# Optimization experiments

Measured on AMD Instinct MI355X. Metric: run time of the kernel, lower is better.

## Reference

```python
import jax, jax.numpy as jnp
import numpy as np
import math

B, S, H, D = 8, 4096, 768, 64  # batch, seq_len, hidden_dim, head_size


def setup_inputs() -> dict:
    key = jax.random.key(0)
    kx, kk, kq, kv, kbk, kbq, kbv = jax.random.split(key, 7)
    s = 1.0 / math.sqrt(H)
    return {
        "x": jax.random.normal(kx, (B, S, H), dtype=jnp.float32),
        "Wk": jax.random.normal(kk, (H, D), dtype=jnp.float32) * s,
        "bk": jax.random.normal(kbk, (D,), dtype=jnp.float32) * s,
        "Wq": jax.random.normal(kq, (H, D), dtype=jnp.float32) * s,
        "bq": jax.random.normal(kbq, (D,), dtype=jnp.float32) * s,
        "Wv": jax.random.normal(kv, (H, D), dtype=jnp.float32) * s,
        "bv": jax.random.normal(kbv, (D,), dtype=jnp.float32) * s,
    }


def reference(x, Wk, bk, Wq, bq, Wv, bv):
    # projections: [B, S, D]
    k = x @ Wk + bk
    q = x @ Wq + bq
    v = x @ Wv + bv
    # full O(S^2) attention scores, as in the original module
    weight = jnp.einsum("bqd,bkd->bqk", q, k)  # [B, S, S]
    causal = jnp.tril(jnp.ones((S, S), dtype=bool))
    # original masks first, then divides by sqrt(head_size); -inf/sqrt = -inf
    weight = jnp.where(causal, weight, -jnp.inf) / math.sqrt(D)
    weight = jax.nn.softmax(weight, axis=-1)
    # dropout p=0.0 (eval-mode reference): identity
    out = jnp.einsum("bqk,bkd->bqd", weight, v)  # [B, S, D]
    return out
```

## Files before the change

### kernel.cpp

```cpp
#include <hip/hip_runtime.h>
#include <hip/hip_bf16.h>
#include <math.h>

#define B_ 8
#define S_ 4096
#define H_ 768
#define D_ 64

typedef __bf16 bf16;
typedef bf16 bf16x8 __attribute__((ext_vector_type(8)));
typedef bf16 bf16x4 __attribute__((ext_vector_type(4)));
typedef float floatx4 __attribute__((ext_vector_type(4)));
typedef short short4v __attribute__((ext_vector_type(4)));

__device__ __forceinline__ floatx4 mfma16(bf16x4 a, bf16x4 b, floatx4 c) {
#if __has_builtin(__builtin_amdgcn_mfma_f32_16x16x16_bf16)
    return __builtin_amdgcn_mfma_f32_16x16x16_bf16(a, b, c, 0, 0, 0);
#elif __has_builtin(__builtin_amdgcn_mfma_f32_16x16x16bf16_1k)
    return __builtin_amdgcn_mfma_f32_16x16x16bf16_1k(
        __builtin_bit_cast(short4v, a), __builtin_bit_cast(short4v, b), c, 0, 0, 0);
#else
    asm volatile("v_mfma_f32_16x16x16_bf16 %0, %1, %2, %0"
                 : "+v"(c) : "v"(a), "v"(b));
    return c;
#endif
}

__device__ __forceinline__ int sw_off(int r, int chunk) {
    return r * 128 + ((chunk ^ (r & 7)) << 4);
}
__device__ __forceinline__ int sw_elem(int r, int e) {
    return r * 64 + (((e >> 3) ^ (r & 7)) << 3) + (e & 7);
}

__device__ __forceinline__ void dma16(const bf16* gsrc, bf16* ldst) {
    __builtin_amdgcn_global_load_lds(
        (const __attribute__((address_space(1))) unsigned int*)(const void*)gsrc,
        (__attribute__((address_space(3))) unsigned int*)(void*)ldst,
        16, 0, 0);
}

__global__ __launch_bounds__(256) void wtrans_kernel(
    const float* __restrict__ Wq, const float* __restrict__ Wk,
    const float* __restrict__ Wv, bf16* __restrict__ wt)
{
    __shared__ bf16 t_lds[64][72];
    const float* W = (blockIdx.y == 0) ? Wq : (blockIdx.y == 1) ? Wk : Wv;
    bf16* o = wt + ((size_t)blockIdx.y * 12 + blockIdx.x) * 4096;
    const int k0 = blockIdx.x * 64;
    const int tid = threadIdx.x;
    #pragma unroll
    for (int rep = 0; rep < 16; ++rep) {
        int idx = rep * 256 + tid;
        int r = idx >> 6, n = idx & 63;
        t_lds[n][r] = (bf16)W[(size_t)(k0 + r) * D_ + n];
    }
    __syncthreads();
    #pragma unroll
    for (int rep = 0; rep < 16; ++rep) {
        int idx = rep * 256 + tid;
        int n = idx >> 6, kk = idx & 63;
        o[sw_elem(n, kk)] = t_lds[n][kk];
    }
}

__global__ __launch_bounds__(256, 3) void proj_kernel(
    const float* __restrict__ x, const bf16* __restrict__ wt,
    const float* __restrict__ bq, const float* __restrict__ bk,
    const float* __restrict__ bv,
    bf16* __restrict__ qout, bf16* __restrict__ kout, bf16* __restrict__ vtt)
{
    __shared__ bf16 wlds[2][3][4096];

    const int m0   = blockIdx.x * 64;
    const int tid  = threadIdx.x;
    const int lane = tid & 63;
    const int wave = tid >> 6;
    const int quad = lane >> 4;
    const int c    = lane & 15;
    const int mrow = m0 + wave * 16 + c;

    floatx4 acc[3][4] = {};
    const float* xrow = &x[(size_t)mrow * H_ + quad * 8];

    auto loadA = [&](int k0, bf16x8* dst) {
        #pragma unroll
        for (int s = 0; s < 2; ++s) {
            const float* xp = xrow + k0 + s * 32;
            float4 f0 = *(const float4*)xp;
            float4 f1 = *(const float4*)(xp + 4);
            bf16x8 a;
            a[0] = (bf16)f0.x; a[1] = (bf16)f0.y; a[2] = (bf16)f0.z; a[3] = (bf16)f0.w;
            a[4] = (bf16)f1.x; a[5] = (bf16)f1.y; a[6] = (bf16)f1.z; a[7] = (bf16)f1.w;
            dst[s] = a;
        }
    };
    auto stageW = [&](int kt, int buf) {
        #pragma unroll
        for (int w = 0; w < 3; ++w) {
            const bf16* src = wt + (size_t)(w * 12 + kt) * 4096 + wave * 1024 + lane * 8;
            bf16* dst = &wlds[buf][w][wave * 1024];
            dma16(src, dst);
            dma16(src + 512, dst + 512);
        }
    };

    bf16x8 aA[2], aB[2];
    loadA(0, aA); loadA(64, aB);
    stageW(0, 0);

    for (int kt = 0; kt < 12; ++kt) {
        __syncthreads();
        const int cur = kt & 1;
        if (kt < 11) stageW(kt + 1, 1 - cur);
        bf16x8 af[2] = { aA[0], aA[1] };
        aA[0] = aB[0]; aA[1] = aB[1];
        if (kt < 10) loadA((kt + 2) * 64, aB);
        #pragma unroll
        for (int s = 0; s < 2; ++s)
            #pragma unroll
            for (int w = 0; w < 3; ++w)
                #pragma unroll
                for (int tn = 0; tn < 4; ++tn) {
                    bf16x8 bfrag = *(const bf16x8*)
                        ((const char*)&wlds[cur][w][0] + sw_off(tn * 16 + c, s * 4 + quad));
                    acc[w][tn] = __builtin_amdgcn_mfma_f32_16x16x32_bf16(
                        af[s], bfrag, acc[w][tn], 0, 0, 0);
                }
    }

    const int rbase = m0 + wave * 16 + quad * 4;
    const int bb = m0 >> 12;
    const int jt = (m0 & 4095) >> 6;
    const size_t tbase = ((size_t)bb * 64 + jt) * 4096;
    #pragma unroll
    for (int tn = 0; tn < 4; ++tn) {
        const int n = tn * 16 + c;
        float bqv = bq[n];
        #pragma unroll
        for (int r = 0; r < 4; ++r)
            qout[(size_t)(rbase + r) * 128 + n] = (bf16)(acc[0][tn][r] + bqv);
        float bkv = bk[n];
        #pragma unroll
        for (int r = 0; r < 4; ++r) {
            const int sl = (rbase & 63) + r;
            kout[tbase + sw_elem(sl, n)] = (bf16)(acc[1][tn][r] + bkv);
        }
        float bvv = bv[n];
        bf16x4 pk;
        #pragma unroll
        for (int r = 0; r < 4; ++r) pk[r] = (bf16)(acc[2][tn][r] + bvv);
        const int sl0 = (rbase & 63);
        *(bf16x4*)&vtt[tbase + sw_elem(n, sl0)] = pk;
    }
}

__global__ __launch_bounds__(128, 2) void attn_kernel(
    const bf16* __restrict__ q, const bf16* __restrict__ k,
    const bf16* __restrict__ vt, float* __restrict__ out,
    float* __restrict__ opart, float* __restrict__ lpws)
{
    __shared__ bf16 klds[2][4096];
    __shared__ bf16 vlds[2][4096];

    const int tid  = threadIdx.x;
    const int lane = tid & 63;
    const int wave = tid >> 6;
    const int quad = lane >> 4;
    const int c    = lane & 15;
    const int i    = blockIdx.x;
    const int b    = i & 7;

    int qt, j0, jend, half = 0, split = 0;
    if (i < 1024) {
        const int u = i >> 3;
        qt   = 127 - (u >> 1);
        half = u & 1;
        split = 1;
        const int jmax = qt >> 1;
        const int jmid = (jmax + 1) >> 1;
        j0   = half ? jmid : 0;
        jend = half ? jmax : (jmid - 1);
    } else {
        qt   = 63 - ((i - 1024) >> 3);
        j0   = 0;
        jend = qt >> 1;
    }
    const int jmax_diag = qt >> 1;
    const int qrow = qt * 32 + wave * 16;
    const float cl = 0.18033688011112042f;
    const float M2 = 16.0f;

    const bf16* ktile0 = k  + (size_t)b * 64 * 4096;
    const bf16* vtile0 = vt + (size_t)b * 64 * 4096;

    auto stage = [&](const bf16* gsrc, bf16* ldst) {
        const bf16* s = gsrc + wave * 2048 + lane * 8;
        bf16* d = ldst + wave * 2048;
        #pragma unroll
        for (int n = 0; n < 4; ++n) dma16(s + n * 512, d + n * 512);
    };

    bf16x8 qf[2];
    #pragma unroll
    for (int s = 0; s < 2; ++s)
        qf[s] = *(const bf16x8*)
            &q[(size_t)(b * S_ + qrow + c) * 128 + s * 32 + quad * 8];

    floatx4 acc_o[4] = {};
    float lsum = 0.f;

    stage(ktile0 + (size_t)j0 * 4096, klds[j0 & 1]);
    stage(vtile0 + (size_t)j0 * 4096, vlds[j0 & 1]);

    #pragma unroll 1
    for (int j = j0; j <= jend; ++j) {
        __syncthreads();
        const int cur = j & 1;
        if (j < jend) {
            stage(ktile0 + (size_t)(j + 1) * 4096, klds[1 - cur]);
            stage(vtile0 + (size_t)(j + 1) * 4096, vlds[1 - cur]);
        }

        floatx4 sa[4] = {};
        #pragma unroll
        for (int s = 0; s < 2; ++s)
            #pragma unroll
            for (int tn = 0; tn < 4; ++tn) {
                bf16x8 kf = *(const bf16x8*)
                    ((const char*)&klds[cur][0] + sw_off(tn * 16 + c, s * 4 + quad));
                sa[tn] = __builtin_amdgcn_mfma_f32_16x16x32_bf16(kf, qf[s], sa[tn], 0, 0, 0);
            }

        bf16x4 vfr[4][4];
        #pragma unroll
        for (int td = 0; td < 4; ++td)
            #pragma unroll
            for (int tn = 0; tn < 4; ++tn)
                vfr[td][tn] = *(const bf16x4*)
                    &vlds[cur][sw_elem(td * 16 + c, tn * 16 + quad * 4)];

        if (j == jmax_diag) {
            #pragma unroll
            for (int tn = 0; tn < 4; ++tn) {
                const int kvb = j * 64 + tn * 16 + quad * 4;
                #pragma unroll
                for (int r = 0; r < 4; ++r)
                    if (kvb + r > qrow + c) sa[tn][r] = -INFINITY;
            }
        }

        #pragma unroll
        for (int tn = 0; tn < 4; ++tn)
            #pragma unroll
            for (int r = 0; r < 4; ++r) {
                float p = __builtin_amdgcn_exp2f(fmaf(sa[tn][r], cl, -M2));
                sa[tn][r] = p;
                lsum += p;
            }

        #pragma unroll
        for (int tn = 0; tn < 4; ++tn) {
            bf16x4 pb;
            #pragma unroll
            for (int r = 0; r < 4; ++r) pb[r] = (bf16)sa[tn][r];
            #pragma unroll
            for (int td = 0; td < 4; ++td)
                acc_o[td] = mfma16(vfr[td][tn], pb, acc_o[td]);
        }
    }

    lsum += __shfl_xor(lsum, 16);
    lsum += __shfl_xor(lsum, 32);

    if (!split) {
        const float rl = 1.0f / lsum;
        #pragma unroll
        for (int td = 0; td < 4; ++td) {
            floatx4 v = acc_o[td] * rl;
            *(float4*)&out[(size_t)(b * S_ + qrow + c) * 64 + td * 16 + quad * 4]
                = *(float4*)&v;
        }
    } else {
        const int tile = qt - 64;
        const int row  = wave * 16 + c;
        float* op = opart + ((((size_t)half * 8 + b) * 64 + tile) * 32) * 64;
        #pragma unroll
        for (int td = 0; td < 4; ++td)
            *(float4*)&op[row * 64 + td * 16 + quad * 4] = *(float4*)&acc_o[td];
        if (quad == 0)
            lpws[(((size_t)half * 8 + b) * 64 + tile) * 32 + row] = lsum;
    }
}

__global__ __launch_bounds__(256) void combine_kernel(
    const float* __restrict__ opart, const float* __restrict__ lpws,
    float* __restrict__ out)
{
    const int b    = blockIdx.x & 7;
    const int tile = blockIdx.x >> 3;
    const int tid  = threadIdx.x;
    const int row  = tid >> 3;
    const int c8   = (tid & 7) * 8;

    const size_t ti = ((size_t)b * 64 + tile) * 32 + row;
    const float rl = 1.0f / (lpws[ti] + lpws[(size_t)8 * 64 * 32 + ti]);

    const size_t oa = (((size_t)b * 64 + tile) * 32 + row) * 64 + c8;
    const size_t ob = (size_t)8 * 64 * 32 * 64 + oa;
    const size_t oo = (size_t)(b * S_ + (64 + tile) * 32 + row) * 64 + c8;
    #pragma unroll
    for (int h = 0; h < 2; ++h) {
        float4 a = *(const float4*)&opart[oa + h * 4];
        float4 bb = *(const float4*)&opart[ob + h * 4];
        float4 o;
        o.x = (a.x + bb.x) * rl; o.y = (a.y + bb.y) * rl;
        o.z = (a.z + bb.z) * rl; o.w = (a.w + bb.w) * rl;
        *(float4*)&out[oo + h * 4] = o;
    }
}

extern "C" void kernel_launch(void* const* d_in, const int* in_sizes, int n_in,
                              void* d_out, int out_size, void* d_ws, size_t ws_size,
                              hipStream_t stream) {
    const float* x  = (const float*)d_in[0];
    const float* Wk = (const float*)d_in[1];
    const float* bk = (const float*)d_in[2];
    const float* Wq = (const float*)d_in[3];
    const float* bq = (const float*)d_in[4];
    const float* Wv = (const float*)d_in[5];
    const float* bv = (const float*)d_in[6];
    float* out = (float*)d_out;

    bf16* q_ws  = (bf16*)d_out;
    bf16* k_ws  = (bf16*)d_ws;
    bf16* vt_ws = k_ws + (size_t)B_ * S_ * D_;
    bf16* wt_ws = vt_ws + (size_t)B_ * S_ * D_;
    float* opart = (float*)(wt_ws + 3 * 12 * 4096);
    float* lpws  = opart + (size_t)2 * 8 * 64 * 32 * 64;

    wtrans_kernel<<<dim3(H_ / 64, 3), 256, 0, stream>>>(Wq, Wk, Wv, wt_ws);
    proj_kernel<<<dim3(B_ * S_ / 64), 256, 0, stream>>>(
        x, wt_ws, bq, bk, bv, q_ws, k_ws, vt_ws);
    attn_kernel<<<dim3(1536), 128, 0, stream>>>(q_ws, k_ws, vt_ws, out, opart, lpws);
    combine_kernel<<<dim3(512), 256, 0, stream>>>(opart, lpws, out);
}
```

Baseline: 216.1 us.

## Stage x tiles via LDS DMA with triple-stage pipeline and N-split waves in projection

The projection kernel now copies x tiles into swizzled LDS with global_load_lds DMA instead of per-thread register loads, and prefetches two k-steps ahead using explicit vmcnt waits and raw barriers. Work is redistributed so each wave covers all 64 rows but only 3 of the 12 output column tiles, which lets the W fragments be reused across row groups. The change aims to hide global load latency and cut redundant W fragment reads from LDS. In exchange, LDS use per block grows, occupancy is lowered to 2 blocks, and the fp32 to bf16 conversion now runs on LDS reads.

Result: no change. 214.8 us (median of 2 runs) (-0.6%).

```diff
diff --git a/kernel.cpp b/kernel.cpp
--- a/kernel.cpp
+++ b/kernel.cpp
@@ -12,6 +12,9 @@
 typedef bf16 bf16x4 __attribute__((ext_vector_type(4)));
 typedef float floatx4 __attribute__((ext_vector_type(4)));
 typedef short short4v __attribute__((ext_vector_type(4)));
+
+#define S_WAITCNT_VM(N) asm volatile("s_waitcnt vmcnt(" #N ")" ::: "memory")
+#define S_BARRIER()     asm volatile("s_barrier" ::: "memory")
 
 __device__ __forceinline__ floatx4 mfma16(bf16x4 a, bf16x4 b, floatx4 c) {
 #if __has_builtin(__builtin_amdgcn_mfma_f32_16x16x16_bf16)
@@ -33,10 +36,10 @@
     return r * 64 + (((e >> 3) ^ (r & 7)) << 3) + (e & 7);
 }
 
-__device__ __forceinline__ void dma16(const bf16* gsrc, bf16* ldst) {
+__device__ __forceinline__ void dma16(const void* gsrc, void* ldst) {
     __builtin_amdgcn_global_load_lds(
-        (const __attribute__((address_space(1))) unsigned int*)(const void*)gsrc,
-        (__attribute__((address_space(3))) unsigned int*)(void*)ldst,
+        (const __attribute__((address_space(1))) unsigned int*)gsrc,
+        (__attribute__((address_space(3))) unsigned int*)ldst,
         16, 0, 0);
 }
 
@@ -64,94 +67,105 @@
     }
 }
 
-__global__ __launch_bounds__(256, 3) void proj_kernel(
+__global__ __launch_bounds__(256, 2) void proj_kernel(
     const float* __restrict__ x, const bf16* __restrict__ wt,
     const float* __restrict__ bq, const float* __restrict__ bk,
     const float* __restrict__ bv,
     bf16* __restrict__ qout, bf16* __restrict__ kout, bf16* __restrict__ vtt)
 {
-    __shared__ bf16 wlds[2][3][4096];
-
-    const int m0   = blockIdx.x * 64;
+    __shared__ bf16  wlds[2][3][4096];
+    __shared__ float xlds[2][4096];
+
     const int tid  = threadIdx.x;
     const int lane = tid & 63;
     const int wave = tid >> 6;
     const int quad = lane >> 4;
     const int c    = lane & 15;
-    const int mrow = m0 + wave * 16 + c;
-
-    floatx4 acc[3][4] = {};
-    const float* xrow = &x[(size_t)mrow * H_ + quad * 8];
-
-    auto loadA = [&](int k0, bf16x8* dst) {
-        #pragma unroll
-        for (int s = 0; s < 2; ++s) {
-            const float* xp = xrow + k0 + s * 32;
-            float4 f0 = *(const float4*)xp;
-            float4 f1 = *(const float4*)(xp + 4);
-            bf16x8 a;
-            a[0] = (bf16)f0.x; a[1] = (bf16)f0.y; a[2] = (bf16)f0.z; a[3] = (bf16)f0.w;
-            a[4] = (bf16)f1.x; a[5] = (bf16)f1.y; a[6] = (bf16)f1.z; a[7] = (bf16)f1.w;
-            dst[s] = a;
-        }
-    };
-    auto stageW = [&](int kt, int buf) {
+    const int m0   = blockIdx.x * 64;
+
+    auto stageAll = [&](int kt, int buf) {
         #pragma unroll
         for (int w = 0; w < 3; ++w) {
             const bf16* src = wt + (size_t)(w * 12 + kt) * 4096 + wave * 1024 + lane * 8;
-            bf16* dst = &wlds[buf][w][wave * 1024];
+            bf16* dst = &wlds[buf][w][wave * 1024 + lane * 8];
             dma16(src, dst);
             dma16(src + 512, dst + 512);
         }
+        #pragma unroll
+        for (int rep = 0; rep < 4; ++rep) {
+            const int ci  = rep * 256 + tid;
+            const int row = ci >> 4;
+            const int l   = (ci & 15) ^ (row & 15);
+            const char* src = (const char*)x
+                + ((size_t)(m0 + row) * H_ + kt * 64) * 4 + l * 16;
+            dma16(src, (char*)&xlds[buf][0] + ci * 16);
+        }
     };
 
-    bf16x8 aA[2], aB[2];
-    loadA(0, aA); loadA(64, aB);
-    stageW(0, 0);
+    floatx4 acc[4][3] = {};
+
+    stageAll(0, 0);
+    stageAll(1, 1);
 
     for (int kt = 0; kt < 12; ++kt) {
-        __syncthreads();
+        if (kt < 11) { S_WAITCNT_VM(10); } else { S_WAITCNT_VM(0); }
+        S_BARRIER();
         const int cur = kt & 1;
-        if (kt < 11) stageW(kt + 1, 1 - cur);
-        bf16x8 af[2] = { aA[0], aA[1] };
-        aA[0] = aB[0]; aA[1] = aB[1];
-        if (kt < 10) loadA((kt + 2) * 64, aB);
-        #pragma unroll
-        for (int s = 0; s < 2; ++s)
-            #pragma unroll
-            for (int w = 0; w < 3; ++w)
-                #pragma unroll
-                for (int tn = 0; tn < 4; ++tn) {
-                    bf16x8 bfrag = *(const bf16x8*)
-                        ((const char*)&wlds[cur][w][0] + sw_off(tn * 16 + c, s * 4 + quad));
-                    acc[w][tn] = __builtin_amdgcn_mfma_f32_16x16x32_bf16(
-                        af[s], bfrag, acc[w][tn], 0, 0, 0);
-                }
-    }
-
-    const int rbase = m0 + wave * 16 + quad * 4;
+        #pragma unroll
+        for (int s = 0; s < 2; ++s) {
+            bf16x8 bfrag[3];
+            #pragma unroll
+            for (int t = 0; t < 3; ++t) {
+                const int g = wave * 3 + t, w = g >> 2, tn = g & 3;
+                bfrag[t] = *(const bf16x8*)
+                    ((const char*)&wlds[cur][w][0] + sw_off(tn * 16 + c, s * 4 + quad));
+            }
+            #pragma unroll
+            for (int mg = 0; mg < 4; ++mg) {
+                const int row = mg * 16 + c;
+                const int lc  = s * 8 + quad * 2;
+                const char* xb = (const char*)&xlds[cur][0] + row * 256;
+                float4 f0 = *(const float4*)(xb + ((lc       ^ (row & 15)) << 4));
+                float4 f1 = *(const float4*)(xb + (((lc + 1) ^ (row & 15)) << 4));
+                bf16x8 af;
+                af[0] = (bf16)f0.x; af[1] = (bf16)f0.y; af[2] = (bf16)f0.z; af[3] = (bf16)f0.w;
+                af[4] = (bf16)f1.x; af[5] = (bf16)f1.y; af[6] = (bf16)f1.z; af[7] = (bf16)f1.w;
+                #pragma unroll
+                for (int t = 0; t < 3; ++t)
+                    acc[mg][t] = __builtin_amdgcn_mfma_f32_16x16x32_bf16(
+                        af, bfrag[t], acc[mg][t], 0, 0, 0);
+            }
+        }
+        S_BARRIER();
+        if (kt < 10) stageAll(kt + 2, cur);
+    }
+
     const int bb = m0 >> 12;
     const int jt = (m0 & 4095) >> 6;
     const size_t tbase = ((size_t)bb * 64 + jt) * 4096;
     #pragma unroll
-    for (int tn = 0; tn < 4; ++tn) {
+    for (int t = 0; t < 3; ++t) {
+        const int g = wave * 3 + t, w = g >> 2, tn = g & 3;
         const int n = tn * 16 + c;
-        float bqv = bq[n];
-        #pragma unroll
-        for (int r = 0; r < 4; ++r)
-            qout[(size_t)(rbase + r) * 128 + n] = (bf16)(acc[0][tn][r] + bqv);
-        float bkv = bk[n];
-        #pragma unroll
-        for (int r = 0; r < 4; ++r) {
-            const int sl = (rbase & 63) + r;
-            kout[tbase + sw_elem(sl, n)] = (bf16)(acc[1][tn][r] + bkv);
-        }
-        float bvv = bv[n];
-        bf16x4 pk;
-        #pragma unroll
-        for (int r = 0; r < 4; ++r) pk[r] = (bf16)(acc[2][tn][r] + bvv);
-        const int sl0 = (rbase & 63);
-        *(bf16x4*)&vtt[tbase + sw_elem(n, sl0)] = pk;
+        const float bias = (w == 0 ? bq : w == 1 ? bk : bv)[n];
+        #pragma unroll
+        for (int mg = 0; mg < 4; ++mg) {
+            const int sl0 = mg * 16 + quad * 4;
+            if (w == 0) {
+                #pragma unroll
+                for (int r = 0; r < 4; ++r)
+                    qout[(size_t)(m0 + sl0 + r) * 128 + n] = (bf16)(acc[mg][t][r] + bias);
+            } else if (w == 1) {
+                #pragma unroll
+                for (int r = 0; r < 4; ++r)
+                    kout[tbase + sw_elem(sl0 + r, n)] = (bf16)(acc[mg][t][r] + bias);
+            } else {
+                bf16x4 pk;
+                #pragma unroll
+                for (int r = 0; r < 4; ++r) pk[r] = (bf16)(acc[mg][t][r] + bias);
+                *(bf16x4*)&vtt[tbase + sw_elem(n, sl0)] = pk;
+            }
+        }
     }
 }
 
```
